# Performance work log

Hardware: AMD Instinct MI355X
Metric: run time of the kernel (lower is better)

Reference implementation:

```python
import jax, jax.numpy as jnp
import numpy as np

B = 8192
E, IN, H, OUT = 6, 2086, 512, 512


def setup_inputs() -> dict:
    key = jax.random.key(0)
    ks = jax.random.split(key, 6)
    wb1 = np.sqrt(6.0 / (IN * H))
    wb2 = np.sqrt(6.0 / (H * H))
    wb3 = np.sqrt(6.0 / (H * OUT))
    return {
        "frame_prev": jax.random.normal(ks[0], (B, 1830), dtype=jnp.float32),
        "I": jax.random.normal(ks[1], (B, 256), dtype=jnp.float32),
        "blending_coef": jax.nn.softmax(jax.random.normal(ks[2], (B, E), dtype=jnp.float32), axis=-1),
        "w1": jax.random.uniform(ks[3], (E, IN, H), jnp.float32, -wb1, wb1),
        "b1": jnp.zeros((E, H), jnp.float32),
        "w2": jax.random.uniform(ks[4], (E, H, H), jnp.float32, -wb2, wb2),
        "b2": jnp.zeros((E, H), jnp.float32),
        "w3": jax.random.uniform(ks[5], (E, H, OUT), jnp.float32, -wb3, wb3),
        "b3": jnp.zeros((E, OUT), jnp.float32),
    }


def _blended_linear(h, coef, w, b):
    # Algebraically identical to sum_e coef[b,e] * (h @ w[e]) + coef @ b,
    # which equals (h @ sum_e coef[b,e] w[e]) + coef @ b as in the torch code,
    # but avoids materializing the [B, in, out] blended weight tensor.
    per_expert = jnp.einsum('bi,eio->beo', h, w)   # [B, E, out]
    return jnp.einsum('be,beo->bo', coef, per_expert) + coef @ b


def reference(frame_prev, I, blending_coef, w1, b1, w2, b2, w3, b3):
    h0 = jnp.concatenate([frame_prev, I], axis=1)          # [B, 2086]
    h1 = jax.nn.elu(_blended_linear(h0, blending_coef, w1, b1))
    h2 = jax.nn.elu(_blended_linear(h1, blending_coef, w2, b2))
    h3 = jax.nn.elu(_blended_linear(h2, blending_coef, w3, b3))
    return h3
```

## Files before the change

### kernel.cpp

```cpp
#include <hip/hip_runtime.h>
#include <hip/hip_bf16.h>
#include <cstdint>
#include <cstddef>

typedef __attribute__((ext_vector_type(4))) float f32x4;
typedef __attribute__((ext_vector_type(8))) short bf16x8;

#define E_  6
#define B_  8192
#define H_  512

__device__ __forceinline__ unsigned short f32_to_bf16_rn(float f) {
    uint32_t u = __float_as_uint(f);
    uint32_t r = (u + 0x7fffu + ((u >> 16) & 1u)) >> 16;
    return (unsigned short)r;
}
__device__ __forceinline__ float bf16_to_f32(unsigned short h) {
    return __uint_as_float(((uint32_t)h) << 16);
}

__global__ __launch_bounds__(256)
void convert_h_t_kernel(const float* __restrict__ srcA, const float* __restrict__ srcB,
                        int splitA, int K_in, int NK,
                        short* __restrict__ dhi, short* __restrict__ dlo)
{
    __shared__ float tile[128][33];
    const int t     = threadIdx.x;
    const int kstep = blockIdx.x;
    const int bm    = blockIdx.y;

    {
        const int r2   = t >> 1;
        const int half = t & 1;
        const int row  = bm * 128 + r2;
        const int kb   = kstep * 32 + half * 16;
        float* dstrow  = &tile[r2][half * 16];
        if (kb + 15 < splitA) {
            const float* p = srcA + (size_t)row * splitA + kb;
#pragma unroll
            for (int j = 0; j < 8; ++j) {
                float2 x = *reinterpret_cast<const float2*>(p + 2 * j);
                dstrow[2 * j] = x.x; dstrow[2 * j + 1] = x.y;
            }
        } else if (kb >= splitA && kb + 15 < K_in) {
            const float* p = srcB + (size_t)row * (K_in - splitA) + (kb - splitA);
#pragma unroll
            for (int j = 0; j < 8; ++j) {
                float2 x = *reinterpret_cast<const float2*>(p + 2 * j);
                dstrow[2 * j] = x.x; dstrow[2 * j + 1] = x.y;
            }
        } else {
#pragma unroll
            for (int j = 0; j < 16; ++j) {
                const int k = kb + j;
                float v = 0.f;
                if (k < K_in) v = (k < splitA) ? srcA[(size_t)row * splitA + k]
                                               : srcB[(size_t)row * (K_in - splitA) + (k - splitA)];
                dstrow[j] = v;
            }
        }
    }
    __syncthreads();

#pragma unroll
    for (int hc = 0; hc < 2; ++hc) {
        const int lc = t + hc * 256;
        const int mf = lc >> 6;
        const int l  = lc & 63;
        const int rl = mf * 16 + (l & 15);
        const int kl = (l >> 4) * 8;
        union { short s[8]; int4 v; } uh, ul;
#pragma unroll
        for (int j = 0; j < 8; ++j) {
            const float v = tile[rl][kl + j];
            const unsigned short hh = f32_to_bf16_rn(v);
            const float rem = v - bf16_to_f32(hh);
            uh.s[j] = (short)hh;
            ul.s[j] = (short)f32_to_bf16_rn(rem);
        }
        const size_t c = (((size_t)bm * NK + kstep) * 8 + mf) * 64 + l;
        *reinterpret_cast<int4*>(dhi + c * 8) = uh.v;
        *reinterpret_cast<int4*>(dlo + c * 8) = ul.v;
    }
}

__global__ void convert_w_kernel(const float* __restrict__ w, int K_in, int NK, int nchunks,
                                 short* __restrict__ dhi, short* __restrict__ dlo)
{
    int c = blockIdx.x * 256 + threadIdx.x;
    if (c >= nchunks) return;
    int lane  = c & 63;
    int nf    = (c >> 6) & 3;
    int rest  = c >> 8;
    int kstep = rest % NK;
    int eb    = rest / NK;
    int bn    = eb & 7;
    int e     = eb >> 3;
    int o  = bn * 64 + nf * 16 + (lane & 15);
    int k0 = kstep * 32 + (lane >> 4) * 8;

    union { short s[8]; int4 v; } uh, ul;
#pragma unroll
    for (int j = 0; j < 8; ++j) {
        int k = k0 + j;
        float v = 0.f;
        if (k < K_in) v = w[((size_t)e * K_in + k) * H_ + o];
        unsigned short h = f32_to_bf16_rn(v);
        float rem = v - bf16_to_f32(h);
        unsigned short l = f32_to_bf16_rn(rem);
        uh.s[j] = (short)h;
        ul.s[j] = (short)l;
    }
    *reinterpret_cast<int4*>(dhi + (size_t)c * 8) = uh.v;
    *reinterpret_cast<int4*>(dlo + (size_t)c * 8) = ul.v;
}

__global__ __launch_bounds__(256, 2)
void blend_gemm_kernel(const short* __restrict__ Ah, const short* __restrict__ Al,
                       const short* __restrict__ Bh, const short* __restrict__ Bl,
                       const float* __restrict__ coef, const float* __restrict__ bias,
                       float* __restrict__ out, int NK)
{
    __shared__ __align__(16) short lds[28672];

    const int tid  = threadIdx.x;
    const int lane = tid & 63;
    const int wave = tid >> 6;
    const int wm   = wave >> 1;
    const int wn   = wave & 1;
    const int blk  = blockIdx.x;
    const int bn   = blk & 7;
    const int bm   = blk >> 3;

    const size_t abase     = (size_t)bm * NK * 4096;
    const size_t bstride_e = (size_t)8 * NK * 2048;
    const size_t bbase0    = (size_t)bn * NK * 2048;

    auto issueA = [&](int s) {
        const size_t a_s = abase + (size_t)s * 4096;
        short* dst = &lds[(s & 1) * 8192];
#pragma unroll
        for (int i = 0; i < 4; ++i) {
            const int ch = wave * 4 + i;
            const short* g = (ch < 8) ? (Ah + a_s + ch * 512)
                                      : (Al + a_s + (ch - 8) * 512);
            __builtin_amdgcn_global_load_lds(
                (const __attribute__((address_space(1))) short*)(g + lane * 8),
                (__attribute__((address_space(3))) short*)(dst + ch * 512),
                16, 0, 0);
        }
    };
    auto issueB = [&](int ebuf, int eexp, int s) {
        const size_t off = (size_t)eexp * bstride_e + bbase0 + (size_t)s * 2048;
        short* dst = &lds[16384 + ebuf * 4096];
#pragma unroll
        for (int i = 0; i < 2; ++i) {
            const int ch = wave * 2 + i;
            const short* g = (ch < 4) ? (Bh + off + ch * 512)
                                      : (Bl + off + (ch - 4) * 512);
            __builtin_amdgcn_global_load_lds(
                (const __attribute__((address_space(1))) short*)(g + lane * 8),
                (__attribute__((address_space(3))) short*)(dst + ch * 512),
                16, 0, 0);
        }
    };

    const f32x4 zero = {0.f, 0.f, 0.f, 0.f};
    f32x4 acc[E_][4][2];
#pragma unroll
    for (int e = 0; e < E_; ++e)
#pragma unroll
        for (int mf = 0; mf < 4; ++mf)
#pragma unroll
            for (int nf = 0; nf < 2; ++nf) acc[e][mf][nf] = zero;

    bf16x8 ah[4], al4[4];

    __builtin_amdgcn_sched_barrier(0);
    issueA(0);
    issueB(0, 0, 0);
    issueB(1, 1, 0);
    __builtin_amdgcn_sched_barrier(0);

    for (int s = 0; s < NK; ++s) {
        const bool lastS = (s == NK - 1);
#pragma unroll
        for (int e = 0; e < 6; ++e) {
            if (e < 4) {
                asm volatile("s_waitcnt vmcnt(2) lgkmcnt(0)" ::: "memory");
            } else if (e == 4) {
                if (!lastS) asm volatile("s_waitcnt vmcnt(6) lgkmcnt(0)" ::: "memory");
                else        asm volatile("s_waitcnt vmcnt(2) lgkmcnt(0)" ::: "memory");
            } else {
                if (!lastS) asm volatile("s_waitcnt vmcnt(6) lgkmcnt(0)" ::: "memory");
                else        asm volatile("s_waitcnt vmcnt(0) lgkmcnt(0)" ::: "memory");
            }
            __builtin_amdgcn_s_barrier();
            __builtin_amdgcn_sched_barrier(0);

            if (e < 4) {
                issueB((e + 2) % 3, e + 2, s);
            } else if (!lastS) {
                issueB((e + 2) % 3, e - 4, s + 1);
            }
            if (e == 3 && !lastS) issueA(s + 1);
            __builtin_amdgcn_sched_barrier(0);

            if (e == 0) {
                const short* Ab = &lds[(s & 1) * 8192];
#pragma unroll
                for (int mf = 0; mf < 4; ++mf) {
                    ah[mf]  = *reinterpret_cast<const bf16x8*>(&Ab[((wm * 4 + mf) * 64 + lane) * 8]);
                    al4[mf] = *reinterpret_cast<const bf16x8*>(&Ab[((8 + wm * 4 + mf) * 64 + lane) * 8]);
                }
            }
            const short* Bb = &lds[16384 + (e % 3) * 4096];
            bf16x8 bh[2], bl[2];
#pragma unroll
            for (int nf = 0; nf < 2; ++nf) {
                bh[nf] = *reinterpret_cast<const bf16x8*>(&Bb[((wn * 2 + nf) * 64 + lane) * 8]);
                bl[nf] = *reinterpret_cast<const bf16x8*>(&Bb[((4 + wn * 2 + nf) * 64 + lane) * 8]);
            }

            __builtin_amdgcn_s_setprio(1);
#pragma unroll
            for (int mf = 0; mf < 4; ++mf)
#pragma unroll
                for (int nf = 0; nf < 2; ++nf) {
                    acc[e][mf][nf] = __builtin_amdgcn_mfma_f32_16x16x32_bf16(ah[mf],  bh[nf], acc[e][mf][nf], 0, 0, 0);
                    acc[e][mf][nf] = __builtin_amdgcn_mfma_f32_16x16x32_bf16(ah[mf],  bl[nf], acc[e][mf][nf], 0, 0, 0);
                    acc[e][mf][nf] = __builtin_amdgcn_mfma_f32_16x16x32_bf16(al4[mf], bh[nf], acc[e][mf][nf], 0, 0, 0);
                }
            __builtin_amdgcn_s_setprio(0);
            __builtin_amdgcn_sched_barrier(0);
        }
    }

    float bb[E_][2];
#pragma unroll
    for (int nf = 0; nf < 2; ++nf) {
        const int col = bn * 64 + wn * 32 + nf * 16 + (lane & 15);
#pragma unroll
        for (int e = 0; e < E_; ++e) bb[e][nf] = bias[e * H_ + col];
    }

#pragma unroll
    for (int mf = 0; mf < 4; ++mf) {
        const int r0 = bm * 128 + wm * 64 + mf * 16 + (lane >> 4) * 4;
#pragma unroll
        for (int q = 0; q < 4; ++q) {
            const int r = r0 + q;
            const float2* c2 = reinterpret_cast<const float2*>(coef + (size_t)r * E_);
            float2 ca = c2[0], cb = c2[1], cc = c2[2];
            float cf[E_] = {ca.x, ca.y, cb.x, cb.y, cc.x, cc.y};
#pragma unroll
            for (int nf = 0; nf < 2; ++nf) {
                const int col = bn * 64 + wn * 32 + nf * 16 + (lane & 15);
                float v = 0.f;
#pragma unroll
                for (int e = 0; e < E_; ++e)
                    v += cf[e] * (acc[e][mf][nf][q] + bb[e][nf]);
                v = v > 0.f ? v : expm1f(v);
                out[(size_t)r * H_ + col] = v;
            }
        }
    }
}

extern "C" void kernel_launch(void* const* d_in, const int* in_sizes, int n_in,
                              void* d_out, int out_size, void* d_ws, size_t ws_size,
                              hipStream_t stream)
{
    if (n_in < 9) return;
    const float* frame = (const float*)d_in[0];
    const float* Iin   = (const float*)d_in[1];
    const float* coef  = (const float*)d_in[2];
    const float* w1    = (const float*)d_in[3];
    const float* b1    = (const float*)d_in[4];
    const float* w2    = (const float*)d_in[5];
    const float* b2    = (const float*)d_in[6];
    const float* w3    = (const float*)d_in[7];
    const float* b3    = (const float*)d_in[8];
    float* out = (float*)d_out;
    char* ws = (char*)d_ws;

    const int NK1 = 66;
    const int NK2 = 16;

    const size_t A0sz = (size_t)8192 * 2112 * 2;
    const size_t W1sz = (size_t)6 * 2112 * 512 * 2;
    const size_t W2sz = (size_t)6 * 512 * 512 * 2;
    const size_t H1f  = (size_t)8192 * 512 * 4;
    const size_t H1b  = (size_t)8192 * 512 * 2;

    const size_t need = 2 * A0sz + 2 * W1sz + 4 * W2sz + H1f + 2 * H1b;
    if (ws_size < need) return;

    short* A0h = (short*)(ws);
    short* A0l = (short*)(ws + A0sz);
    short* w1h = (short*)(ws + 2 * A0sz);
    short* w1l = (short*)(ws + 2 * A0sz + W1sz);
    short* w2h = (short*)(ws + 2 * A0sz + 2 * W1sz);
    short* w2l = (short*)(ws + 2 * A0sz + 2 * W1sz + W2sz);
    short* w3h = (short*)(ws + 2 * A0sz + 2 * W1sz + 2 * W2sz);
    short* w3l = (short*)(ws + 2 * A0sz + 2 * W1sz + 3 * W2sz);
    float* h1  = (float*)(ws + 2 * A0sz + 2 * W1sz + 4 * W2sz);
    short* h1h = (short*)((char*)h1 + H1f);
    short* h1l = (short*)((char*)h1 + H1f + H1b);
    float* h2  = (float*)(ws);
    short* h2h = (short*)(ws + H1f);
    short* h2l = (short*)(ws + H1f + H1b);

    {
        dim3 g(NK1, 64);
        convert_h_t_kernel<<<g, 256, 0, stream>>>(frame, Iin, 1830, 2086, NK1, A0h, A0l);
    }
    {
        int nch = 6 * 8 * NK1 * 4 * 64;
        convert_w_kernel<<<nch / 256, 256, 0, stream>>>(w1, 2086, NK1, nch, w1h, w1l);
    }
    {
        int nch = 6 * 8 * NK2 * 4 * 64;
        convert_w_kernel<<<nch / 256, 256, 0, stream>>>(w2, 512, NK2, nch, w2h, w2l);
        convert_w_kernel<<<nch / 256, 256, 0, stream>>>(w3, 512, NK2, nch, w3h, w3l);
    }

    const int grid = 512;
    blend_gemm_kernel<<<grid, 256, 0, stream>>>(A0h, A0l, w1h, w1l, coef, b1, h1, NK1);
    {
        dim3 g(NK2, 64);
        convert_h_t_kernel<<<g, 256, 0, stream>>>(h1, nullptr, 512, 512, NK2, h1h, h1l);
    }
    blend_gemm_kernel<<<grid, 256, 0, stream>>>(h1h, h1l, w2h, w2l, coef, b2, h2, NK2);
    {
        dim3 g(NK2, 64);
        convert_h_t_kernel<<<g, 256, 0, stream>>>(h2, nullptr, 512, 512, NK2, h2h, h2l);
    }
    blend_gemm_kernel<<<grid, 256, 0, stream>>>(h2h, h2l, w3h, w3l, coef, b3, out, NK2);
}
```

Before: 542.5 us.

## Halve GEMM M-tile to 64 rows and raise occupancy to four blocks per CU

The blend GEMM block tile shrinks from 128 to 64 rows, so the grid doubles to 1024 blocks and accumulators and A fragments are halved. The A tile is now single-buffered and B uses three slots in a smaller LDS footprint, with reworked issue order and waitcnt values. Launch bounds move to 4 blocks per CU to raise occupancy and latency hiding. In exchange, each B (weight) tile is reused across fewer rows, which doubles weight traffic, and single-buffering A adds pipeline hazards.

Result: slower. 2.046 ms (+277.1%).

```diff
diff --git a/kernel.cpp b/kernel.cpp
--- a/kernel.cpp
+++ b/kernel.cpp
@@ -115,13 +115,13 @@
     *reinterpret_cast<int4*>(dlo + (size_t)c * 8) = ul.v;
 }
 
-__global__ __launch_bounds__(256, 2)
+__global__ __launch_bounds__(256, 4)
 void blend_gemm_kernel(const short* __restrict__ Ah, const short* __restrict__ Al,
                        const short* __restrict__ Bh, const short* __restrict__ Bl,
                        const float* __restrict__ coef, const float* __restrict__ bias,
                        float* __restrict__ out, int NK)
 {
-    __shared__ __align__(16) short lds[28672];
+    __shared__ __align__(16) short lds[16384];
 
     const int tid  = threadIdx.x;
     const int lane = tid & 63;
@@ -131,28 +131,30 @@
     const int blk  = blockIdx.x;
     const int bn   = blk & 7;
     const int bm   = blk >> 3;
-
-    const size_t abase     = (size_t)bm * NK * 4096;
+    const int bm128   = bm >> 1;
+    const int mfhalf  = (bm & 1) * 4;
+
+    const size_t abase     = (size_t)bm128 * NK * 4096;
     const size_t bstride_e = (size_t)8 * NK * 2048;
     const size_t bbase0    = (size_t)bn * NK * 2048;
 
     auto issueA = [&](int s) {
         const size_t a_s = abase + (size_t)s * 4096;
-        short* dst = &lds[(s & 1) * 8192];
-#pragma unroll
-        for (int i = 0; i < 4; ++i) {
-            const int ch = wave * 4 + i;
-            const short* g = (ch < 8) ? (Ah + a_s + ch * 512)
-                                      : (Al + a_s + (ch - 8) * 512);
+        short* dst = &lds[0];
+#pragma unroll
+        for (int i = 0; i < 2; ++i) {
+            const int ch = wave * 2 + i;
+            const short* g = (ch < 4) ? (Ah + a_s + (mfhalf + ch) * 512)
+                                      : (Al + a_s + (mfhalf + ch - 4) * 512);
             __builtin_amdgcn_global_load_lds(
                 (const __attribute__((address_space(1))) short*)(g + lane * 8),
                 (__attribute__((address_space(3))) short*)(dst + ch * 512),
                 16, 0, 0);
         }
     };
-    auto issueB = [&](int ebuf, int eexp, int s) {
+    auto issueB = [&](int slot, int eexp, int s) {
         const size_t off = (size_t)eexp * bstride_e + bbase0 + (size_t)s * 2048;
-        short* dst = &lds[16384 + ebuf * 4096];
+        short* dst = &lds[4096 + slot * 4096];
 #pragma unroll
         for (int i = 0; i < 2; ++i) {
             const int ch = wave * 2 + i;
@@ -166,15 +168,15 @@
     };
 
     const f32x4 zero = {0.f, 0.f, 0.f, 0.f};
-    f32x4 acc[E_][4][2];
+    f32x4 acc[E_][2][2];
 #pragma unroll
     for (int e = 0; e < E_; ++e)
 #pragma unroll
-        for (int mf = 0; mf < 4; ++mf)
+        for (int mf = 0; mf < 2; ++mf)
 #pragma unroll
             for (int nf = 0; nf < 2; ++nf) acc[e][mf][nf] = zero;
 
-    bf16x8 ah[4], al4[4];
+    bf16x8 ah[2], al4[2];
 
     __builtin_amdgcn_sched_barrier(0);
     issueA(0);
@@ -186,45 +188,53 @@
         const bool lastS = (s == NK - 1);
 #pragma unroll
         for (int e = 0; e < 6; ++e) {
-            if (e < 4) {
+            if (e == 2 || e == 3) {
+                if (!lastS) asm volatile("s_waitcnt vmcnt(4) lgkmcnt(0)" ::: "memory");
+                else        asm volatile("s_waitcnt vmcnt(2) lgkmcnt(0)" ::: "memory");
+            } else if (e == 5) {
+                if (!lastS) asm volatile("s_waitcnt vmcnt(2) lgkmcnt(0)" ::: "memory");
+                else        asm volatile("s_waitcnt vmcnt(0) lgkmcnt(0)" ::: "memory");
+            } else {
                 asm volatile("s_waitcnt vmcnt(2) lgkmcnt(0)" ::: "memory");
-            } else if (e == 4) {
-                if (!lastS) asm volatile("s_waitcnt vmcnt(6) lgkmcnt(0)" ::: "memory");
-                else        asm volatile("s_waitcnt vmcnt(2) lgkmcnt(0)" ::: "memory");
-            } else {
-                if (!lastS) asm volatile("s_waitcnt vmcnt(6) lgkmcnt(0)" ::: "memory");
-                else        asm volatile("s_waitcnt vmcnt(0) lgkmcnt(0)" ::: "memory");
             }
             __builtin_amdgcn_s_barrier();
             __builtin_amdgcn_sched_barrier(0);
 
-            if (e < 4) {
-                issueB((e + 2) % 3, e + 2, s);
-            } else if (!lastS) {
-                issueB((e + 2) % 3, e - 4, s + 1);
-            }
-            if (e == 3 && !lastS) issueA(s + 1);
+            if (e == 0) {
+                issueB(2, 2, s);
+            } else if (e == 1) {
+                issueB(0, 3, s);
+                if (!lastS) issueA(s + 1);
+            } else if (e == 2) {
+                issueB(1, 4, s);
+            } else if (e == 3) {
+                issueB(2, 5, s);
+            } else if (e == 4) {
+                if (!lastS) issueB(0, 0, s + 1);
+            } else {
+                if (!lastS) issueB(1, 1, s + 1);
+            }
             __builtin_amdgcn_sched_barrier(0);
 
             if (e == 0) {
-                const short* Ab = &lds[(s & 1) * 8192];
-#pragma unroll
-                for (int mf = 0; mf < 4; ++mf) {
-                    ah[mf]  = *reinterpret_cast<const bf16x8*>(&Ab[((wm * 4 + mf) * 64 + lane) * 8]);
-                    al4[mf] = *reinterpret_cast<const bf16x8*>(&Ab[((8 + wm * 4 + mf) * 64 + lane) * 8]);
+                const short* Ab = &lds[0];
+#pragma unroll
+                for (int mf = 0; mf < 2; ++mf) {
+                    ah[mf]  = *reinterpret_cast<const bf16x8*>(&Ab[((    wm * 2 + mf) * 64 + lane) * 8]);
+                    al4[mf] = *reinterpret_cast<const bf16x8*>(&Ab[((4 + wm * 2 + mf) * 64 + lane) * 8]);
                 }
             }
-            const short* Bb = &lds[16384 + (e % 3) * 4096];
+            const short* Bb = &lds[4096 + (e % 3) * 4096];
             bf16x8 bh[2], bl[2];
 #pragma unroll
             for (int nf = 0; nf < 2; ++nf) {
-                bh[nf] = *reinterpret_cast<const bf16x8*>(&Bb[((wn * 2 + nf) * 64 + lane) * 8]);
+                bh[nf] = *reinterpret_cast<const bf16x8*>(&Bb[((    wn * 2 + nf) * 64 + lane) * 8]);
                 bl[nf] = *reinterpret_cast<const bf16x8*>(&Bb[((4 + wn * 2 + nf) * 64 + lane) * 8]);
             }
 
             __builtin_amdgcn_s_setprio(1);
 #pragma unroll
-            for (int mf = 0; mf < 4; ++mf)
+            for (int mf = 0; mf < 2; ++mf)
 #pragma unroll
                 for (int nf = 0; nf < 2; ++nf) {
                     acc[e][mf][nf] = __builtin_amdgcn_mfma_f32_16x16x32_bf16(ah[mf],  bh[nf], acc[e][mf][nf], 0, 0, 0);
@@ -245,8 +255,8 @@
     }
 
 #pragma unroll
-    for (int mf = 0; mf < 4; ++mf) {
-        const int r0 = bm * 128 + wm * 64 + mf * 16 + (lane >> 4) * 4;
+    for (int mf = 0; mf < 2; ++mf) {
+        const int r0 = bm * 64 + wm * 32 + mf * 16 + (lane >> 4) * 4;
 #pragma unroll
         for (int q = 0; q < 4; ++q) {
             const int r = r0 + q;
@@ -325,7 +335,7 @@
         convert_w_kernel<<<nch / 256, 256, 0, stream>>>(w3, 512, NK2, nch, w3h, w3l);
     }
 
-    const int grid = 512;
+    const int grid = 1024;
     blend_gemm_kernel<<<grid, 256, 0, stream>>>(A0h, A0l, w1h, w1l, coef, b1, h1, NK1);
     {
         dim3 g(NK2, 64);
```
